# Optimization experiments

Measured on AMD Instinct MI355X. Metric: run time of the kernel, lower is better.

The kernel has to match this reference:

```python
import jax, jax.numpy as jnp
import numpy as np

E4M3 = jnp.float8_e4m3fn  # forward fp8 dtype (HYBRID recipe fwd)

def fp8_qdq(x, fp8_dtype):
    # quantize (scale=1) to fp8 then dequantize back: models precision loss
    return x.astype(fp8_dtype).astype(x.dtype)

def setup_inputs() -> dict:
    key = jax.random.key(0)
    k1, k2 = jax.random.split(key)
    tokens, d_in, units = 4096, 1024, 4096
    x = jax.random.normal(k1, (tokens, d_in), dtype=jnp.float32)
    # kernel_initializer default: RandomNormal(mean=0.0, stddev=0.023)
    kernel = jax.random.normal(k2, (d_in, units), dtype=jnp.float32) * 0.023
    bias = jnp.zeros((units,), dtype=jnp.float32)
    return {"x": x, "kernel": kernel, "bias": bias}

def reference(x, kernel, bias):
    # fp8 quantize/dequantize prologue on activations and weights
    xq = fp8_qdq(x, E4M3)          # [tokens, d_in]
    kq = fp8_qdq(kernel, E4M3)     # [d_in, units]
    out = jnp.matmul(xq, kq) + bias  # [tokens, units]
    # gelu approximate=True (tanh approximation)
    return jax.nn.gelu(out, approximate=True)
```

## Files before the change

### kernel.cpp

```cpp
#include <hip/hip_runtime.h>
#include <hip/hip_bf16.h>

typedef float f32x4 __attribute__((ext_vector_type(4)));
typedef long  l2    __attribute__((ext_vector_type(2)));

__device__ __forceinline__ void gld16(const void* g, void* l) {
    __builtin_amdgcn_global_load_lds(
        (const __attribute__((address_space(1))) void*)g,
        (__attribute__((address_space(3))) void*)l,
        16, 0, 0);
}

__device__ __forceinline__ float gelu_tanh(float x) {
    float u = 0.7978845608028654f * x * (1.0f + 0.044715f * x * x);
    float e = __expf(2.0f * u);
    float t = 1.0f - 2.0f / (e + 1.0f);
    return 0.5f * x * (1.0f + t);
}


__global__ __launch_bounds__(256) void quantA_kernel(
        const float* __restrict__ in, unsigned char* __restrict__ out,
        int n4, int K) {
    int i = blockIdx.x * 256 + threadIdx.x;
    if (i >= n4) return;
    float4 v = reinterpret_cast<const float4*>(in)[i];
    int pk = 0;
    pk = __builtin_amdgcn_cvt_pk_fp8_f32(v.x, v.y, pk, false);
    pk = __builtin_amdgcn_cvt_pk_fp8_f32(v.z, v.w, pk, true);
    const long k4 = (long)i * 4;
    const int  row = (int)(k4 / K);
    const int  k   = (int)(k4 % K);
    const int  o   = k & 63;
    const int  g   = (o & 31) >> 3;
    const int  s   = (o & 7) + ((o >> 5) & 1) * 8;
    const int  c   = g ^ ((row >> 1) & 3);
    *reinterpret_cast<unsigned int*>(
        out + (long)row * K + (k & ~63) + (c << 4) + s) = (unsigned int)pk;
}

__global__ __launch_bounds__(256) void quantBT_kernel(
        const float* __restrict__ B, unsigned char* __restrict__ BT,
        int K, int N) {
    __shared__ unsigned char lds[64 * 68];
    const int tid = threadIdx.x;
    const int n0 = blockIdx.x * 64;
    const int k0 = blockIdx.y * 64;

    #pragma unroll
    for (int p = 0; p < 4; ++p) {
        int s = p * 256 + tid;
        int r = s >> 4;
        int c = s & 15;
        float4 v = *reinterpret_cast<const float4*>(
            B + (long)(k0 + r) * N + n0 + c * 4);
        int pk = 0;
        pk = __builtin_amdgcn_cvt_pk_fp8_f32(v.x, v.y, pk, false);
        pk = __builtin_amdgcn_cvt_pk_fp8_f32(v.z, v.w, pk, true);
        *reinterpret_cast<unsigned int*>(&lds[r * 68 + c * 4]) = (unsigned int)pk;
    }
    __syncthreads();
    #pragma unroll
    for (int p = 0; p < 4; ++p) {
        int sidx = p * 256 + tid;
        int n  = sidx >> 4;
        int kg = sidx & 15;
        unsigned int w = 0;
        #pragma unroll
        for (int j = 0; j < 4; ++j)
            w |= (unsigned int)lds[(kg * 4 + j) * 68 + n] << (8 * j);
        const int nn = n0 + n;
        const int o  = kg * 4;
        const int g  = (o & 31) >> 3;
        const int s  = (o & 7) + ((o >> 5) & 1) * 8;
        const int c  = g ^ ((nn >> 1) & 3);
        *reinterpret_cast<unsigned int*>(
            BT + (long)nn * K + k0 + (c << 4) + s) = w;
    }
}

__global__ __launch_bounds__(512, 4) void gemm_fp8_kernel(
        const unsigned char* __restrict__ A,
        const unsigned char* __restrict__ BT,
        const float* __restrict__ bias,
        float* __restrict__ out,
        int M, int N, int K) {
    constexpr int BM = 128, BN = 256, BK = 64;
    __shared__ unsigned char lds[3][(BM + BN) * BK];

    const int tid  = threadIdx.x;
    const int lane = tid & 63;
    const int wid  = tid >> 6;
    const int wm   = wid >> 2;
    const int wn   = wid & 3;

    const int bid = blockIdx.x;
    const int xcd = bid & 7, idx = bid >> 3;
    const int tile_m = (xcd >> 1) * 8 + (idx & 7);
    const int tile_n = (xcd & 1) * 8 + (idx >> 3);
    const int m0 = tile_m * BM, n0 = tile_n * BN;

    const int lrow = lane & 15;
    const int kgrp = lane >> 4;
    const int chunkoff = ((kgrp ^ ((lrow >> 1) & 3)) << 4);

    const int srow   = tid >> 2;
    const int schunk = (tid & 3) << 4;
    const unsigned char* gA = A  + (long)(m0 + srow) * K + schunk;
    const unsigned char* gB = BT + (long)(n0 + srow) * K + schunk;

    const int aBase = (wm * 64 + lrow) * 64 + chunkoff;
    const int bBase = 8192 + (wn * 64 + lrow) * 64 + chunkoff;

    f32x4 acc[4][4] = {};

    const int NT = K / BK;

#define STAGE_A(BB, TT)                                                   \
    gld16(gA + (long)(TT) * BK, &lds[BB][wid * 1024])
#define STAGE_B(BB, H, TT)                                                \
    gld16(gB + (long)(H) * 128 * K + (long)(TT) * BK,                     \
          &lds[BB][8192 + (H) * 8192 + wid * 1024])

#define PHASE_HEAD()                                                      \
    __builtin_amdgcn_sched_barrier(0);                                    \
    __builtin_amdgcn_s_barrier();                                         \
    asm volatile("s_waitcnt lgkmcnt(0)" ::: "memory");                    \
    __builtin_amdgcn_sched_barrier(0);                                    \
    __builtin_amdgcn_s_setprio(1)

#define PHASE_TAIL()                                                      \
    __builtin_amdgcn_s_setprio(0);                                        \
    __builtin_amdgcn_sched_barrier(0);                                    \
    __builtin_amdgcn_s_barrier()

#define MFMA_Q(AI0, BJ0, AR, BR)                                          \
    _Pragma("unroll") for (int ks = 0; ks < 2; ++ks)                      \
    _Pragma("unroll") for (int fi = 0; fi < 2; ++fi)                      \
    _Pragma("unroll") for (int fj = 0; fj < 2; ++fj)                      \
        acc[(AI0) + fi][(BJ0) + fj] =                                     \
            __builtin_amdgcn_mfma_f32_16x16x32_fp8_fp8(                   \
                AR[fi][ks], BR[fj][ks], acc[(AI0) + fi][(BJ0) + fj], 0, 0, 0)

    STAGE_A(0, 0); STAGE_B(0, 0, 0); STAGE_B(0, 1, 0);
    STAGE_A(1, 1); STAGE_B(1, 0, 1); STAGE_B(1, 1, 1);
    asm volatile("s_waitcnt vmcnt(3)" ::: "memory");
    __builtin_amdgcn_sched_barrier(0);
    __builtin_amdgcn_s_barrier();

    int b = 0, b2 = 2;
    for (int t = 0; t < NT; ++t) {
        const unsigned char* sL = &lds[b][0];
        const bool st = (t + 2 < NT);
        l2 a01[2], a23[2], b01[2], b23[2];

        #pragma unroll
        for (int f = 0; f < 2; ++f) {
            a01[f] = *reinterpret_cast<const l2*>(sL + aBase + f * 1024);
            b01[f] = *reinterpret_cast<const l2*>(sL + bBase + f * 1024);
        }
        if (st) { STAGE_A(b2, t + 2); }
        PHASE_HEAD();
        MFMA_Q(0, 0, a01, b01);
        PHASE_TAIL();

        #pragma unroll
        for (int f = 0; f < 2; ++f)
            b23[f] = *reinterpret_cast<const l2*>(sL + bBase + 2048 + f * 1024);
        if (st) { STAGE_B(b2, 0, t + 2); }
        PHASE_HEAD();
        MFMA_Q(0, 2, a01, b23);
        PHASE_TAIL();

        #pragma unroll
        for (int f = 0; f < 2; ++f)
            a23[f] = *reinterpret_cast<const l2*>(sL + aBase + 2048 + f * 1024);
        if (st) { STAGE_B(b2, 1, t + 2); }
        PHASE_HEAD();
        MFMA_Q(2, 0, a23, b01);
        PHASE_TAIL();

        __builtin_amdgcn_s_barrier();
        __builtin_amdgcn_s_setprio(1);
        MFMA_Q(2, 2, a23, b23);
        __builtin_amdgcn_s_setprio(0);
        __builtin_amdgcn_sched_barrier(0);
        if (t < NT - 1) {
            if (st) { asm volatile("s_waitcnt vmcnt(3)" ::: "memory"); }
            else    { asm volatile("s_waitcnt vmcnt(0)" ::: "memory"); }
            __builtin_amdgcn_sched_barrier(0);
            __builtin_amdgcn_s_barrier();
        }
        b  = (b  == 2) ? 0 : b  + 1;
        b2 = (b2 == 2) ? 0 : b2 + 1;
    }

    __syncthreads();
    float* eplds = reinterpret_cast<float*>(&lds[0][0]) + wid * 1088;
    const int  col0   = n0 + wn * 64;
    const long rbase0 = m0 + wm * 64;
    float bv[4];
    #pragma unroll
    for (int bj = 0; bj < 4; ++bj) bv[bj] = bias[col0 + bj * 16 + lrow];

    #pragma unroll
    for (int ai = 0; ai < 4; ++ai) {
        #pragma unroll
        for (int bj = 0; bj < 4; ++bj) {
            #pragma unroll
            for (int r = 0; r < 4; ++r) {
                float xv = acc[ai][bj][r] + bv[bj];
                eplds[(kgrp * 4 + r) * 68 + bj * 16 + lrow] = gelu_tanh(xv);
            }
        }
        #pragma unroll
        for (int s = 0; s < 4; ++s) {
            f32x4 v = *reinterpret_cast<const f32x4*>(
                eplds + (s * 4 + kgrp) * 68 + lrow * 4);
            *reinterpret_cast<f32x4*>(
                out + (rbase0 + ai * 16 + s * 4 + kgrp) * N + col0 + lrow * 4) = v;
        }
    }
#undef STAGE_A
#undef STAGE_B
#undef PHASE_HEAD
#undef PHASE_TAIL
#undef MFMA_Q
}

extern "C" void kernel_launch(void* const* d_in, const int* in_sizes, int n_in,
                              void* d_out, int out_size, void* d_ws, size_t ws_size,
                              hipStream_t stream) {
    const float* x    = (const float*)d_in[0];
    const float* w    = (const float*)d_in[1];
    const float* bias = (const float*)d_in[2];
    float* out = (float*)d_out;

    const int units  = in_sizes[2];
    const int dmodel = in_sizes[1] / units;
    const int tokens = in_sizes[0] / dmodel;

    unsigned char* Aq  = (unsigned char*)d_ws;
    unsigned char* BTq = Aq + (size_t)tokens * dmodel;

    const int n4a = tokens * dmodel / 4;
    quantA_kernel<<<dim3(n4a / 256), dim3(256), 0, stream>>>(
        x, Aq, n4a, dmodel);

    quantBT_kernel<<<dim3(units / 64, dmodel / 64), dim3(256), 0, stream>>>(
        w, BTq, dmodel, units);

    const int nblocks = (tokens / 128) * (units / 256);
    gemm_fp8_kernel<<<dim3(nblocks), dim3(512), 0, stream>>>(
        Aq, BTq, bias, out, tokens, units, dmodel);
}
```

Baseline: 49.09 us.

## Fuse quantization kernels, merge GEMM barrier phases, use nontemporal output stores

```diff
diff --git a/kernel.cpp b/kernel.cpp
--- a/kernel.cpp
+++ b/kernel.cpp
@@ -19,33 +19,34 @@
 }
 
 
-__global__ __launch_bounds__(256) void quantA_kernel(
-        const float* __restrict__ in, unsigned char* __restrict__ out,
-        int n4, int K) {
-    int i = blockIdx.x * 256 + threadIdx.x;
-    if (i >= n4) return;
-    float4 v = reinterpret_cast<const float4*>(in)[i];
-    int pk = 0;
-    pk = __builtin_amdgcn_cvt_pk_fp8_f32(v.x, v.y, pk, false);
-    pk = __builtin_amdgcn_cvt_pk_fp8_f32(v.z, v.w, pk, true);
-    const long k4 = (long)i * 4;
-    const int  row = (int)(k4 / K);
-    const int  k   = (int)(k4 % K);
-    const int  o   = k & 63;
-    const int  g   = (o & 31) >> 3;
-    const int  s   = (o & 7) + ((o >> 5) & 1) * 8;
-    const int  c   = g ^ ((row >> 1) & 3);
-    *reinterpret_cast<unsigned int*>(
-        out + (long)row * K + (k & ~63) + (c << 4) + s) = (unsigned int)pk;
-}
-
-__global__ __launch_bounds__(256) void quantBT_kernel(
-        const float* __restrict__ B, unsigned char* __restrict__ BT,
-        int K, int N) {
+__global__ __launch_bounds__(256) void quant_fused_kernel(
+        const float* __restrict__ x,  unsigned char* __restrict__ Aq,
+        const float* __restrict__ w,  unsigned char* __restrict__ BTq,
+        int nA, int K, int N) {
     __shared__ unsigned char lds[64 * 68];
     const int tid = threadIdx.x;
-    const int n0 = blockIdx.x * 64;
-    const int k0 = blockIdx.y * 64;
+
+    if (blockIdx.x < nA) {
+        int i = blockIdx.x * 256 + tid;
+        float4 v = reinterpret_cast<const float4*>(x)[i];
+        int pk = 0;
+        pk = __builtin_amdgcn_cvt_pk_fp8_f32(v.x, v.y, pk, false);
+        pk = __builtin_amdgcn_cvt_pk_fp8_f32(v.z, v.w, pk, true);
+        const long k4 = (long)i * 4;
+        const int  row = (int)(k4 / K);
+        const int  k   = (int)(k4 % K);
+        const int  o   = k & 63;
+        const int  g   = (o & 31) >> 3;
+        const int  s   = (o & 7) + ((o >> 5) & 1) * 8;
+        const int  c   = g ^ ((row >> 1) & 3);
+        *reinterpret_cast<unsigned int*>(
+            Aq + (long)row * K + (k & ~63) + (c << 4) + s) = (unsigned int)pk;
+        return;
+    }
+
+    const int bid = blockIdx.x - nA;
+    const int n0 = (bid & (N / 64 - 1)) * 64;
+    const int k0 = (bid / (N / 64)) * 64;
 
     #pragma unroll
     for (int p = 0; p < 4; ++p) {
@@ -53,7 +54,7 @@
         int r = s >> 4;
         int c = s & 15;
         float4 v = *reinterpret_cast<const float4*>(
-            B + (long)(k0 + r) * N + n0 + c * 4);
+            w + (long)(k0 + r) * N + n0 + c * 4);
         int pk = 0;
         pk = __builtin_amdgcn_cvt_pk_fp8_f32(v.x, v.y, pk, false);
         pk = __builtin_amdgcn_cvt_pk_fp8_f32(v.z, v.w, pk, true);
@@ -65,17 +66,17 @@
         int sidx = p * 256 + tid;
         int n  = sidx >> 4;
         int kg = sidx & 15;
-        unsigned int w = 0;
+        unsigned int wv = 0;
         #pragma unroll
         for (int j = 0; j < 4; ++j)
-            w |= (unsigned int)lds[(kg * 4 + j) * 68 + n] << (8 * j);
+            wv |= (unsigned int)lds[(kg * 4 + j) * 68 + n] << (8 * j);
         const int nn = n0 + n;
         const int o  = kg * 4;
         const int g  = (o & 31) >> 3;
         const int s  = (o & 7) + ((o >> 5) & 1) * 8;
         const int c  = g ^ ((nn >> 1) & 3);
         *reinterpret_cast<unsigned int*>(
-            BT + (long)nn * K + k0 + (c << 4) + s) = w;
+            BTq + (long)nn * K + k0 + (c << 4) + s) = wv;
     }
 }
 
@@ -122,18 +123,6 @@
     gld16(gB + (long)(H) * 128 * K + (long)(TT) * BK,                     \
           &lds[BB][8192 + (H) * 8192 + wid * 1024])
 
-#define PHASE_HEAD()                                                      \
-    __builtin_amdgcn_sched_barrier(0);                                    \
-    __builtin_amdgcn_s_barrier();                                         \
-    asm volatile("s_waitcnt lgkmcnt(0)" ::: "memory");                    \
-    __builtin_amdgcn_sched_barrier(0);                                    \
-    __builtin_amdgcn_s_setprio(1)
-
-#define PHASE_TAIL()                                                      \
-    __builtin_amdgcn_s_setprio(0);                                        \
-    __builtin_amdgcn_sched_barrier(0);                                    \
-    __builtin_amdgcn_s_barrier()
-
 #define MFMA_Q(AI0, BJ0, AR, BR)                                          \
     _Pragma("unroll") for (int ks = 0; ks < 2; ++ks)                      \
     _Pragma("unroll") for (int fi = 0; fi < 2; ++fi)                      \
@@ -145,7 +134,6 @@
     STAGE_A(0, 0); STAGE_B(0, 0, 0); STAGE_B(0, 1, 0);
     STAGE_A(1, 1); STAGE_B(1, 0, 1); STAGE_B(1, 1, 1);
     asm volatile("s_waitcnt vmcnt(3)" ::: "memory");
-    __builtin_amdgcn_sched_barrier(0);
     __builtin_amdgcn_s_barrier();
 
     int b = 0, b2 = 2;
@@ -154,37 +142,34 @@
         const bool st = (t + 2 < NT);
         l2 a01[2], a23[2], b01[2], b23[2];
 
+        if (st) { STAGE_A(b2, t + 2); STAGE_B(b2, 0, t + 2); }
         #pragma unroll
         for (int f = 0; f < 2; ++f) {
             a01[f] = *reinterpret_cast<const l2*>(sL + aBase + f * 1024);
             b01[f] = *reinterpret_cast<const l2*>(sL + bBase + f * 1024);
-        }
-        if (st) { STAGE_A(b2, t + 2); }
-        PHASE_HEAD();
+            b23[f] = *reinterpret_cast<const l2*>(sL + bBase + 2048 + f * 1024);
+        }
+        __builtin_amdgcn_s_barrier();
+        asm volatile("s_waitcnt lgkmcnt(0)" ::: "memory");
+        __builtin_amdgcn_sched_barrier(0);
+        __builtin_amdgcn_s_setprio(1);
         MFMA_Q(0, 0, a01, b01);
-        PHASE_TAIL();
-
-        #pragma unroll
-        for (int f = 0; f < 2; ++f)
-            b23[f] = *reinterpret_cast<const l2*>(sL + bBase + 2048 + f * 1024);
-        if (st) { STAGE_B(b2, 0, t + 2); }
-        PHASE_HEAD();
         MFMA_Q(0, 2, a01, b23);
-        PHASE_TAIL();
-
+        __builtin_amdgcn_s_setprio(0);
+
+        if (st) { STAGE_B(b2, 1, t + 2); }
         #pragma unroll
         for (int f = 0; f < 2; ++f)
             a23[f] = *reinterpret_cast<const l2*>(sL + aBase + 2048 + f * 1024);
-        if (st) { STAGE_B(b2, 1, t + 2); }
-        PHASE_HEAD();
+        __builtin_amdgcn_s_barrier();
+        asm volatile("s_waitcnt lgkmcnt(0)" ::: "memory");
+        __builtin_amdgcn_sched_barrier(0);
+        __builtin_amdgcn_s_setprio(1);
         MFMA_Q(2, 0, a23, b01);
-        PHASE_TAIL();
-
-        __builtin_amdgcn_s_barrier();
-        __builtin_amdgcn_s_setprio(1);
         MFMA_Q(2, 2, a23, b23);
         __builtin_amdgcn_s_setprio(0);
         __builtin_amdgcn_sched_barrier(0);
+
         if (t < NT - 1) {
             if (st) { asm volatile("s_waitcnt vmcnt(3)" ::: "memory"); }
             else    { asm volatile("s_waitcnt vmcnt(0)" ::: "memory"); }
@@ -217,14 +202,12 @@
         for (int s = 0; s < 4; ++s) {
             f32x4 v = *reinterpret_cast<const f32x4*>(
                 eplds + (s * 4 + kgrp) * 68 + lrow * 4);
-            *reinterpret_cast<f32x4*>(
-                out + (rbase0 + ai * 16 + s * 4 + kgrp) * N + col0 + lrow * 4) = v;
+            __builtin_nontemporal_store(v, reinterpret_cast<f32x4*>(
+                out + (rbase0 + ai * 16 + s * 4 + kgrp) * N + col0 + lrow * 4));
         }
     }
 #undef STAGE_A
 #undef STAGE_B
-#undef PHASE_HEAD
-#undef PHASE_TAIL
 #undef MFMA_Q
 }
 
@@ -243,12 +226,10 @@
     unsigned char* Aq  = (unsigned char*)d_ws;
     unsigned char* BTq = Aq + (size_t)tokens * dmodel;
 
-    const int n4a = tokens * dmodel / 4;
-    quantA_kernel<<<dim3(n4a / 256), dim3(256), 0, stream>>>(
-        x, Aq, n4a, dmodel);
-
-    quantBT_kernel<<<dim3(units / 64, dmodel / 64), dim3(256), 0, stream>>>(
-        w, BTq, dmodel, units);
+    const int nA = tokens * dmodel / 4 / 256;
+    const int nB = (units / 64) * (dmodel / 64);
+    quant_fused_kernel<<<dim3(nA + nB), dim3(256), 0, stream>>>(
+        x, Aq, w, BTq, nA, dmodel, units);
 
     const int nblocks = (tokens / 128) * (units / 256);
     gemm_fp8_kernel<<<dim3(nblocks), dim3(512), 0, stream>>>(
```

New measurement: 46.98 us. -4.3%, faster.
